# Optimization experiments

Measured on AMD Instinct MI355X. Metric: run time of the kernel, lower is better.

Reference implementation:

```python
import jax, jax.numpy as jnp
from jax import lax
import numpy as np

T, B, H, NUM_DATA, IN_DIM = 2048, 256, 128, 4096, 1


def setup_inputs() -> dict:
    key = jax.random.key(0)
    ks = jax.random.split(key, 9)
    s = 1.0 / np.sqrt(H)  # PyTorch LSTM/Linear default init scale
    inp = {
        "input": jax.random.normal(ks[0], (T, B, IN_DIM), dtype=jnp.float32),
        "label": jax.random.randint(ks[1], (B,), 0, NUM_DATA),
        "h0": jnp.zeros((1, NUM_DATA, H), dtype=jnp.float32),
        "W_ih": jax.random.uniform(ks[2], (4 * H, IN_DIM), jnp.float32, -s, s),
        "W_hh": jax.random.uniform(ks[3], (4 * H, H), jnp.float32, -s, s),
        "b_ih": jax.random.uniform(ks[4], (4 * H,), jnp.float32, -s, s),
        "b_hh": jax.random.uniform(ks[5], (4 * H,), jnp.float32, -s, s),
        "W_lin": jax.random.uniform(ks[6], (IN_DIM, H), jnp.float32, -s, s),
        "b_lin": jax.random.uniform(ks[7], (IN_DIM,), jnp.float32, -s, s),
    }
    return inp


def reference(input, label, h0, W_ih, W_hh, b_ih, b_hh, W_lin, b_lin):
    seq_len = input.shape[0]
    num_in_batch = input.shape[1]
    # Gather learned initial hidden state per sequence id (the python cat loop in torch)
    h = h0[0, label]                                   # (B, H)
    c = jnp.zeros_like(h)                              # (B, H)
    y0 = jnp.zeros((num_in_batch, IN_DIM), input.dtype)  # t=0 input is zeros
    b = b_ih + b_hh                                    # (4H,)

    def step(carry, _):
        h, c, x = carry
        gates = x @ W_ih.T + h @ W_hh.T + b            # (B, 4H); torch gate order i,f,g,o
        i, f, g, o = jnp.split(gates, 4, axis=-1)
        i = jax.nn.sigmoid(i)
        f = jax.nn.sigmoid(f)
        g = jnp.tanh(g)
        o = jax.nn.sigmoid(o)
        c = f * c + i * g
        h = o * jnp.tanh(c)
        y = h @ W_lin.T + b_lin                        # (B, 1) -> fed back as next input
        return (h, c, y), y

    _, ys = lax.scan(step, (h, c, y0), None, length=seq_len)
    return ys  # (T, B, 1), matches torch cat of (1, B, 1) along dim 0
```

## Files before the change

kernel.cpp:

```cpp
#include <hip/hip_runtime.h>
#include <math.h>

#define T_STEPS 2048
#define BATCH   256
#define HDIM    128

__device__ __forceinline__ float fast_rcp(float x) { return __builtin_amdgcn_rcpf(x); }
__device__ __forceinline__ float sigmoid_f(float x) { return fast_rcp(1.0f + __expf(-x)); }
__device__ __forceinline__ float tanh_f(float x) {
    float e = __expf(2.0f * x);
    return 1.0f - 2.0f * fast_rcp(e + 1.0f);
}

#define REP8(M) M(0) M(1) M(2) M(3) M(4) M(5) M(6) M(7)

__global__ __launch_bounds__(512, 2)
void lstm_seq_kernel(const int*   __restrict__ label,
                     const float* __restrict__ h0,
                     const float* __restrict__ W_ih,
                     const float* __restrict__ W_hh,
                     const float* __restrict__ b_ih,
                     const float* __restrict__ b_hh,
                     const float* __restrict__ W_lin,
                     const float* __restrict__ b_lin,
                     float*       __restrict__ out)
{
    const int tid   = threadIdx.x;
    const int batch = blockIdx.x;
    const int m     = tid >> 2;
    const int q     = tid & 3;
    const int q8    = q * 8;

    const int ri = m, rf = m + 128, rg = m + 256, ro = m + 384;

    __shared__ __attribute__((aligned(16))) float hist[128 * 144];

    const float4* W4 = (const float4*)W_hh;
    const float4* L4 = (const float4*)W_lin;

    #define DECL_W(i) \
        float4 wi##i = W4[ri * 32 + q8 + (i)]; \
        float4 wf##i = W4[rf * 32 + q8 + (i)]; \
        float4 wg##i = W4[rg * 32 + q8 + (i)]; \
        float4 wo##i = W4[ro * 32 + q8 + (i)];
    REP8(DECL_W)

    const float wih_i = W_ih[ri], wih_f = W_ih[rf];
    const float wih_g = W_ih[rg], wih_o = W_ih[ro];
    const float blin  = b_lin[0];

    const float bi_ = b_ih[ri] + b_hh[ri] + wih_i * blin;
    const float bf_ = b_ih[rf] + b_hh[rf] + wih_f * blin;
    const float bg_ = b_ih[rg] + b_hh[rg] + wih_g * blin;
    const float bo_ = b_ih[ro] + b_hh[ro] + wih_o * blin;

    const float SNEG = -0x1.715476p+0f;
    const float SG   =  0x1.715476p+1f;
    const float sI = bi_ * 0.25f * SNEG;
    const float sF = bf_ * 0.25f * SNEG;
    const float sG_ = bg_ * 0.25f * SG;
    const float sO = bo_ * 0.25f * SNEG;

    const float b0s = (q==0)?sI :(q==1)?sF :(q==2)?sG_:sO;
    const float b1s = (q==0)?sF :(q==1)?sI :(q==2)?sO :sG_;
    const float b2s = (q==0)?sG_:(q==1)?sO :(q==2)?sI :sF;
    const float b3s = (q==0)?sO :(q==1)?sG_:(q==2)?sF :sI;
    const float wihA = (q==0)?wih_i:(q==1)?wih_f:(q==2)?wih_g:wih_o;
    const float wihB = (q==0)?wih_f:(q==1)?wih_i:(q==2)?wih_o:wih_g;
    const float wihC = (q==0)?wih_g:(q==1)?wih_o:(q==2)?wih_i:wih_f;
    const float wihD = (q==0)?wih_o:(q==1)?wih_g:(q==2)?wih_f:wih_i;
    const float sc0 = ( q     == 2) ? SG : SNEG;
    const float sc1 = ((q^1)  == 2) ? SG : SNEG;
    const float sc2 = ((q^2)  == 2) ? SG : SNEG;
    const float sc3 = ((q^3)  == 2) ? SG : SNEG;
    const float caq = (q==2) ? -2.0f : 1.0f;
    const float cbq = (q==2) ?  1.0f : 0.0f;

    #define FOLD_W(i) { float4 lv = L4[q8 + (i)]; \
        wi##i.x = fmaf(wih_i, lv.x, wi##i.x); wi##i.y = fmaf(wih_i, lv.y, wi##i.y); \
        wi##i.z = fmaf(wih_i, lv.z, wi##i.z); wi##i.w = fmaf(wih_i, lv.w, wi##i.w); \
        wf##i.x = fmaf(wih_f, lv.x, wf##i.x); wf##i.y = fmaf(wih_f, lv.y, wf##i.y); \
        wf##i.z = fmaf(wih_f, lv.z, wf##i.z); wf##i.w = fmaf(wih_f, lv.w, wf##i.w); \
        wg##i.x = fmaf(wih_g, lv.x, wg##i.x); wg##i.y = fmaf(wih_g, lv.y, wg##i.y); \
        wg##i.z = fmaf(wih_g, lv.z, wg##i.z); wg##i.w = fmaf(wih_g, lv.w, wg##i.w); \
        wo##i.x = fmaf(wih_o, lv.x, wo##i.x); wo##i.y = fmaf(wih_o, lv.y, wo##i.y); \
        wo##i.z = fmaf(wih_o, lv.z, wo##i.z); wo##i.w = fmaf(wih_o, lv.w, wo##i.w); }
    REP8(FOLD_W)

    const int   lane = tid & 63;
    const int   ya0w = lane + ((lane >> 5) << 2);
    const float wl_a = W_lin[lane];
    const float wl_b = W_lin[lane + 64];
    const int   hword = m + ((m >> 5) << 2);

    float* slotI = &hist[144 * 127];
    if (tid < HDIM) slotI[tid + ((tid >> 5) << 2)] = h0[label[batch] * HDIM + tid];
    __syncthreads();

    float p0 = slotI[ya0w] * wl_a + slotI[ya0w + 72] * wl_b;
    #pragma unroll
    for (int off = 1; off < 64; off <<= 1) p0 += __shfl_xor(p0, off, 64);
    const float y0 = p0 + blin;

    const float cbi = bi_ - wih_i * y0;
    const float cbf = bf_ - wih_f * y0;
    const float cbg = bg_ - wih_g * y0;
    const float cbo = bo_ - wih_o * y0;

    const float4* hq0 = (const float4*)(slotI + 36 * q);
    float ai = 0.f, af = 0.f, ag = 0.f, ao = 0.f;
    #define DOT4(i) { float4 hv = hq0[(i)]; \
        ai = fmaf(hv.x, wi##i.x, ai); ai = fmaf(hv.y, wi##i.y, ai); \
        ai = fmaf(hv.z, wi##i.z, ai); ai = fmaf(hv.w, wi##i.w, ai); \
        af = fmaf(hv.x, wf##i.x, af); af = fmaf(hv.y, wf##i.y, af); \
        af = fmaf(hv.z, wf##i.z, af); af = fmaf(hv.w, wf##i.w, af); \
        ag = fmaf(hv.x, wg##i.x, ag); ag = fmaf(hv.y, wg##i.y, ag); \
        ag = fmaf(hv.z, wg##i.z, ag); ag = fmaf(hv.w, wg##i.w, ag); \
        ao = fmaf(hv.x, wo##i.x, ao); ao = fmaf(hv.y, wo##i.y, ao); \
        ao = fmaf(hv.z, wo##i.z, ao); ao = fmaf(hv.w, wo##i.w, ao); }
    REP8(DOT4)
    ai += __shfl_xor(ai, 1, 64); af += __shfl_xor(af, 1, 64);
    ag += __shfl_xor(ag, 1, 64); ao += __shfl_xor(ao, 1, 64);
    ai += __shfl_xor(ai, 2, 64); af += __shfl_xor(af, 2, 64);
    ag += __shfl_xor(ag, 2, 64); ao += __shfl_xor(ao, 2, 64);
    const float iv0 = sigmoid_f(ai + cbi);
    const float fv0 = sigmoid_f(af + cbf);
    const float gv0 = tanh_f  (ag + cbg);
    const float ov0 = sigmoid_f(ao + cbo);
    float c = iv0 * gv0;
    const float hn0 = ov0 * tanh_f(c);
    if (q == 0) hist[hword] = hn0;
    __syncthreads();

    const unsigned histB = (unsigned)(unsigned long long)(&hist[0]);
    const unsigned vR0 = histB + 144u * (unsigned)q;
    const unsigned hW0 = histB + 4u * (unsigned)hword;
    const unsigned vD0 = (unsigned)(144 * q - 4 * hword);
    const unsigned fR0 = histB + 576u * (unsigned)m + 144u * (unsigned)q;
    const unsigned jO0 = 1024u * (unsigned)m;
    const unsigned vO0 = 4u * (unsigned)batch;
    const unsigned off0 = (unsigned)((m + 128 * (q    )) * 512 + q * 128);
    const unsigned off1 = (unsigned)((m + 128 * (q ^ 1)) * 512 + q * 128);
    const unsigned off2 = (unsigned)((m + 128 * (q ^ 2)) * 512 + q * 128);
    const unsigned off3 = (unsigned)((m + 128 * (q ^ 3)) * 512 + q * 128);
    const unsigned offL = (unsigned)(q * 128);

    asm volatile(
        "v_mov_b32 v220, %[b0]\n\t"
        "v_mov_b32 v221, 0\n\t"
        "v_mov_b32 v222, %[b1]\n\t"
        "v_mov_b32 v223, 0\n\t"
        "v_mov_b32 v224, %[b2]\n\t"
        "v_mov_b32 v225, 0\n\t"
        "v_mov_b32 v226, %[b3]\n\t"
        "v_mov_b32 v227, 0\n\t"
        "v_mov_b32 v185, %[blin]\n\t"
        "v_mov_b32 v168, %[c0]\n\t"
        "v_mov_b32 v172, %[vR]\n\t"
        "v_mov_b32 v174, %[hW]\n\t"
        "v_mov_b32 v186, %[vD]\n\t"
        "v_mov_b32 v184, %[fR]\n\t"
        "v_mov_b32 v171, %[jO]\n\t"
        "v_mov_b32 v176, %[vO]\n\t"
        "s_mov_b32 s26, 0x11111111\n\t"
        "s_mov_b32 s27, 0x11111111\n\t"
        "global_load_dwordx4 v[32:35], %[off0], %[whh] offset:0\n\t"
        "global_load_dwordx4 v[36:39], %[off0], %[whh] offset:16\n\t"
        "global_load_dwordx4 v[40:43], %[off0], %[whh] offset:32\n\t"
        "global_load_dwordx4 v[44:47], %[off0], %[whh] offset:48\n\t"
        "global_load_dwordx4 v[48:51], %[off0], %[whh] offset:64\n\t"
        "global_load_dwordx4 v[52:55], %[off0], %[whh] offset:80\n\t"
        "global_load_dwordx4 v[56:59], %[off0], %[whh] offset:96\n\t"
        "global_load_dwordx4 v[60:63], %[off0], %[whh] offset:112\n\t"
        "global_load_dwordx4 v[64:67], %[off1], %[whh] offset:0\n\t"
        "global_load_dwordx4 v[68:71], %[off1], %[whh] offset:16\n\t"
        "global_load_dwordx4 v[72:75], %[off1], %[whh] offset:32\n\t"
        "global_load_dwordx4 v[76:79], %[off1], %[whh] offset:48\n\t"
        "global_load_dwordx4 v[80:83], %[off1], %[whh] offset:64\n\t"
        "global_load_dwordx4 v[84:87], %[off1], %[whh] offset:80\n\t"
        "global_load_dwordx4 v[88:91], %[off1], %[whh] offset:96\n\t"
        "global_load_dwordx4 v[92:95], %[off1], %[whh] offset:112\n\t"
        "global_load_dwordx4 v[96:99], %[off2], %[whh] offset:0\n\t"
        "global_load_dwordx4 v[100:103], %[off2], %[whh] offset:16\n\t"
        "global_load_dwordx4 v[104:107], %[off2], %[whh] offset:32\n\t"
        "global_load_dwordx4 v[108:111], %[off2], %[whh] offset:48\n\t"
        "global_load_dwordx4 v[112:115], %[off2], %[whh] offset:64\n\t"
        "global_load_dwordx4 v[116:119], %[off2], %[whh] offset:80\n\t"
        "global_load_dwordx4 v[120:123], %[off2], %[whh] offset:96\n\t"
        "global_load_dwordx4 v[124:127], %[off2], %[whh] offset:112\n\t"
        "global_load_dwordx4 v[128:131], %[off3], %[whh] offset:0\n\t"
        "global_load_dwordx4 v[132:135], %[off3], %[whh] offset:16\n\t"
        "global_load_dwordx4 v[136:139], %[off3], %[whh] offset:32\n\t"
        "global_load_dwordx4 v[140:143], %[off3], %[whh] offset:48\n\t"
        "global_load_dwordx4 v[144:147], %[off3], %[whh] offset:64\n\t"
        "global_load_dwordx4 v[148:151], %[off3], %[whh] offset:80\n\t"
        "global_load_dwordx4 v[152:155], %[off3], %[whh] offset:96\n\t"
        "global_load_dwordx4 v[156:159], %[off3], %[whh] offset:112\n\t"
        "global_load_dwordx4 v[188:191], %[offL], %[wlin] offset:0\n\t"
        "global_load_dwordx4 v[192:195], %[offL], %[wlin] offset:16\n\t"
        "global_load_dwordx4 v[196:199], %[offL], %[wlin] offset:32\n\t"
        "global_load_dwordx4 v[200:203], %[offL], %[wlin] offset:48\n\t"
        "global_load_dwordx4 v[204:207], %[offL], %[wlin] offset:64\n\t"
        "global_load_dwordx4 v[208:211], %[offL], %[wlin] offset:80\n\t"
        "global_load_dwordx4 v[212:215], %[offL], %[wlin] offset:96\n\t"
        "global_load_dwordx4 v[216:219], %[offL], %[wlin] offset:112\n\t"
        "s_waitcnt vmcnt(0)\n\t"
        ".set K_I, 0\n"
        ".rept 32\n"
        " v_fma_f32 v[32+K_I],  %[wA], v[188+K_I], v[32+K_I]\n"
        " v_fma_f32 v[64+K_I],  %[wB], v[188+K_I], v[64+K_I]\n"
        " v_fma_f32 v[96+K_I],  %[wC], v[188+K_I], v[96+K_I]\n"
        " v_fma_f32 v[128+K_I], %[wD], v[188+K_I], v[128+K_I]\n"
        " .set K_I, K_I+1\n"
        ".endr\n"
        ".set K_I, 0\n"
        ".rept 32\n"
        " v_mul_f32 v[32+K_I],  %[sc0], v[32+K_I]\n"
        " v_mul_f32 v[64+K_I],  %[sc1], v[64+K_I]\n"
        " v_mul_f32 v[96+K_I],  %[sc2], v[96+K_I]\n"
        " v_mul_f32 v[128+K_I], %[sc3], v[128+K_I]\n"
        " .set K_I, K_I+1\n"
        ".endr\n"
        "s_movk_i32 s24, 1\n\t"
        "1:\n\t"
        "ds_read_b128 v[0:3],   v172\n\t"
        "ds_read_b128 v[4:7],   v172 offset:16\n\t"
        "ds_read_b128 v[8:11],  v172 offset:32\n\t"
        "ds_read_b128 v[12:15], v172 offset:48\n\t"
        "ds_read_b128 v[16:19], v172 offset:64\n\t"
        "ds_read_b128 v[20:23], v172 offset:80\n\t"
        "ds_read_b128 v[24:27], v172 offset:96\n\t"
        "ds_read_b128 v[28:31], v172 offset:112\n\t"
        "s_waitcnt lgkmcnt(6)\n\t"
        "v_pk_fma_f32 v[160:161], v[0:1], v[32:33], v[220:221]\n\t"
        "v_pk_fma_f32 v[162:163], v[0:1], v[64:65], v[222:223]\n\t"
        "v_pk_fma_f32 v[164:165], v[0:1], v[96:97], v[224:225]\n\t"
        "v_pk_fma_f32 v[166:167], v[0:1], v[128:129], v[226:227]\n\t"
        ".set K_I, 2\n"
        ".rept 3\n"
        " v_pk_fma_f32 v[160:161], v[K_I:K_I+1], v[32+K_I:33+K_I], v[160:161]\n"
        " v_pk_fma_f32 v[162:163], v[K_I:K_I+1], v[64+K_I:65+K_I], v[162:163]\n"
        " v_pk_fma_f32 v[164:165], v[K_I:K_I+1], v[96+K_I:97+K_I], v[164:165]\n"
        " v_pk_fma_f32 v[166:167], v[K_I:K_I+1], v[128+K_I:129+K_I], v[166:167]\n"
        " .set K_I, K_I+2\n"
        ".endr\n"
        "s_waitcnt lgkmcnt(4)\n\t"
        ".rept 4\n"
        " v_pk_fma_f32 v[160:161], v[K_I:K_I+1], v[32+K_I:33+K_I], v[160:161]\n"
        " v_pk_fma_f32 v[162:163], v[K_I:K_I+1], v[64+K_I:65+K_I], v[162:163]\n"
        " v_pk_fma_f32 v[164:165], v[K_I:K_I+1], v[96+K_I:97+K_I], v[164:165]\n"
        " v_pk_fma_f32 v[166:167], v[K_I:K_I+1], v[128+K_I:129+K_I], v[166:167]\n"
        " .set K_I, K_I+2\n"
        ".endr\n"
        "s_waitcnt lgkmcnt(2)\n\t"
        ".rept 4\n"
        " v_pk_fma_f32 v[160:161], v[K_I:K_I+1], v[32+K_I:33+K_I], v[160:161]\n"
        " v_pk_fma_f32 v[162:163], v[K_I:K_I+1], v[64+K_I:65+K_I], v[162:163]\n"
        " v_pk_fma_f32 v[164:165], v[K_I:K_I+1], v[96+K_I:97+K_I], v[164:165]\n"
        " v_pk_fma_f32 v[166:167], v[K_I:K_I+1], v[128+K_I:129+K_I], v[166:167]\n"
        " .set K_I, K_I+2\n"
        ".endr\n"
        "s_waitcnt lgkmcnt(0)\n\t"
        ".rept 4\n"
        " v_pk_fma_f32 v[160:161], v[K_I:K_I+1], v[32+K_I:33+K_I], v[160:161]\n"
        " v_pk_fma_f32 v[162:163], v[K_I:K_I+1], v[64+K_I:65+K_I], v[162:163]\n"
        " v_pk_fma_f32 v[164:165], v[K_I:K_I+1], v[96+K_I:97+K_I], v[164:165]\n"
        " v_pk_fma_f32 v[166:167], v[K_I:K_I+1], v[128+K_I:129+K_I], v[166:167]\n"
        " .set K_I, K_I+2\n"
        ".endr\n"
        "v_add_f32 v160, v160, v161\n\t"
        "v_add_f32 v161, v162, v163\n\t"
        "v_add_f32 v164, v164, v165\n\t"
        "v_add_f32 v165, v166, v167\n\t"
        "s_nop 1\n\t"
        "v_add_f32_dpp v160, v161, v160 quad_perm:[1,0,3,2] row_mask:0xf bank_mask:0xf\n\t"
        "v_add_f32_dpp v164, v165, v164 quad_perm:[1,0,3,2] row_mask:0xf bank_mask:0xf\n\t"
        "v_add_u32 v174, 0x240, v174\n\t"
        "v_add_u32 v172, v174, v186\n\t"
        "s_nop 1\n\t"
        "v_add_f32_dpp v160, v164, v160 quad_perm:[2,3,0,1] row_mask:0xf bank_mask:0xf\n\t"
        "s_nop 3\n\t"
        "v_exp_f32 v160, v160\n\t"
        "s_nop 1\n\t"
        "v_add_f32 v160, 1.0, v160\n\t"
        "v_rcp_f32 v160, v160\n\t"
        "s_nop 1\n\t"
        "v_fma_f32 v166, %[ca], v160, %[cb]\n\t"
        "s_nop 3\n\t"
        "v_mul_f32_dpp v161, v166, v166 quad_perm:[2,3,0,1] row_mask:0xf bank_mask:0xf\n\t"
        "v_mov_b32_dpp v162, v166 quad_perm:[1,0,3,2] row_mask:0xf bank_mask:0xf\n\t"
        "v_mov_b32_dpp v165, v166 quad_perm:[3,3,3,3] row_mask:0xf bank_mask:0xf\n\t"
        "s_nop 2\n\t"
        "v_fma_f32 v168, v162, v168, v161\n\t"
        "v_mul_f32 v163, 0x4038aa3b, v168\n\t"
        "v_exp_f32 v163, v163\n\t"
        "s_nop 1\n\t"
        "v_add_f32 v163, 1.0, v163\n\t"
        "v_rcp_f32 v163, v163\n\t"
        "s_nop 1\n\t"
        "v_fma_f32 v163, -2.0, v163, 1.0\n\t"
        "v_mul_f32 v169, v165, v163\n\t"
        "s_mov_b64 s[22:23], exec\n\t"
        "s_mov_b64 exec, s[26:27]\n\t"
        "ds_write_b32 v174, v169\n\t"
        "s_mov_b64 exec, s[22:23]\n\t"
        "s_waitcnt lgkmcnt(0)\n\t"
        "s_barrier\n\t"
        "s_and_b32 s20, s24, 127\n\t"
        "s_cmp_lg_u32 s20, 127\n\t"
        "s_cbranch_scc1 3f\n\t"
        "v_add_u32 v174, 0xfffee000, v174\n\t"
        "ds_read_b128 v[0:3],   v184\n\t"
        "ds_read_b128 v[4:7],   v184 offset:16\n\t"
        "ds_read_b128 v[8:11],  v184 offset:32\n\t"
        "ds_read_b128 v[12:15], v184 offset:48\n\t"
        "ds_read_b128 v[16:19], v184 offset:64\n\t"
        "ds_read_b128 v[20:23], v184 offset:80\n\t"
        "ds_read_b128 v[24:27], v184 offset:96\n\t"
        "ds_read_b128 v[28:31], v184 offset:112\n\t"
        "v_mov_b32 v164, 0\n\t"
        "s_waitcnt lgkmcnt(0)\n\t"
        ".set K_I, 0\n"
        ".rept 32\n"
        " v_fma_f32 v164, v[0+K_I], v[188+K_I], v164\n"
        " .set K_I, K_I+1\n"
        ".endr\n"
        "s_nop 1\n\t"
        "v_add_f32_dpp v164, v164, v164 quad_perm:[1,0,3,2] row_mask:0xf bank_mask:0xf\n\t"
        "s_nop 1\n\t"
        "v_add_f32_dpp v164, v164, v164 quad_perm:[2,3,0,1] row_mask:0xf bank_mask:0xf\n\t"
        "v_add_f32 v164, v164, v185\n\t"
        "v_add_u32 v170, v176, v171\n\t"
        "s_mov_b64 s[22:23], exec\n\t"
        "s_mov_b64 exec, s[26:27]\n\t"
        "global_store_dword v170, v164, %[outp]\n\t"
        "s_mov_b64 exec, s[22:23]\n\t"
        "v_add_u32 v176, 0x20000, v176\n\t"
        "s_barrier\n\t"
        "3:\n\t"
        "s_add_i32 s24, s24, 1\n\t"
        "s_cmp_lt_i32 s24, 2048\n\t"
        "s_cbranch_scc1 1b\n\t"
        :
        : [off0]"v"(off0), [off1]"v"(off1), [off2]"v"(off2), [off3]"v"(off3),
          [offL]"v"(offL), [whh]"s"(W_hh), [wlin]"s"(W_lin), [outp]"s"(out),
          [wA]"v"(wihA), [wB]"v"(wihB), [wC]"v"(wihC), [wD]"v"(wihD),
          [b0]"v"(b0s), [b1]"v"(b1s), [b2]"v"(b2s), [b3]"v"(b3s),
          [sc0]"v"(sc0), [sc1]"v"(sc1), [sc2]"v"(sc2), [sc3]"v"(sc3),
          [ca]"v"(caq), [cb]"v"(cbq),
          [blin]"s"(blin), [c0]"v"(c),
          [vR]"v"(vR0), [hW]"v"(hW0), [vD]"v"(vD0), [fR]"v"(fR0),
          [jO]"v"(jO0), [vO]"s"(vO0)
        : "memory", "scc", "vcc", "s20","s21","s22","s23","s24","s25","s26","s27",
          "v0","v1","v2","v3","v4","v5","v6","v7","v8","v9",
          "v10","v11","v12","v13","v14","v15","v16","v17","v18","v19",
          "v20","v21","v22","v23","v24","v25","v26","v27","v28","v29",
          "v30","v31","v32","v33","v34","v35","v36","v37","v38","v39",
          "v40","v41","v42","v43","v44","v45","v46","v47","v48","v49",
          "v50","v51","v52","v53","v54","v55","v56","v57","v58","v59",
          "v60","v61","v62","v63","v64","v65","v66","v67","v68","v69",
          "v70","v71","v72","v73","v74","v75","v76","v77","v78","v79",
          "v80","v81","v82","v83","v84","v85","v86","v87","v88","v89",
          "v90","v91","v92","v93","v94","v95","v96","v97","v98","v99",
          "v100","v101","v102","v103","v104","v105","v106","v107","v108","v109",
          "v110","v111","v112","v113","v114","v115","v116","v117","v118","v119",
          "v120","v121","v122","v123","v124","v125","v126","v127","v128","v129",
          "v130","v131","v132","v133","v134","v135","v136","v137","v138","v139",
          "v140","v141","v142","v143","v144","v145","v146","v147","v148","v149",
          "v150","v151","v152","v153","v154","v155","v156","v157","v158","v159",
          "v160","v161","v162","v163","v164","v165","v166","v167","v168","v169",
          "v170","v171","v172","v173","v174","v175","v176","v177","v178","v179",
          "v180","v181","v182","v183","v184","v185","v186","v187","v188","v189",
          "v190","v191","v192","v193","v194","v195","v196","v197","v198","v199",
          "v200","v201","v202","v203","v204","v205","v206","v207","v208","v209",
          "v210","v211","v212","v213","v214","v215","v216","v217","v218","v219",
          "v220","v221","v222","v223","v224","v225","v226","v227");
}

extern "C" void kernel_launch(void* const* d_in, const int* in_sizes, int n_in,
                              void* d_out, int out_size, void* d_ws, size_t ws_size,
                              hipStream_t stream) {
    const int*   label = (const int*)  d_in[1];
    const float* h0    = (const float*)d_in[2];
    const float* W_ih  = (const float*)d_in[3];
    const float* W_hh  = (const float*)d_in[4];
    const float* b_ih  = (const float*)d_in[5];
    const float* b_hh  = (const float*)d_in[6];
    const float* W_lin = (const float*)d_in[7];
    const float* b_lin = (const float*)d_in[8];
    float* out = (float*)d_out;

    lstm_seq_kernel<<<dim3(BATCH), dim3(512), 0, stream>>>(
        label, h0, W_ih, W_hh, b_ih, b_hh, W_lin, b_lin, out);
}
```

Measured before the change: 1.126 ms.

## Split each hidden row's dot product across two lane groups with 1024-thread blocks

The block grows from 512 to 1024 threads. Each of the 4 lanes per hidden row now owns a 16-element slice of the K dimension instead of 32, and the extra row_ror:8 DPP step completes the reduction. This halves the per-thread recurrent dot-product chain and register use per step, and frees enough registers to drop the persistent W_lin copy, which is reloaded from global memory at every 128-step flush instead. The cost is an extra cross-lane reduction stage, a barrier across 16 waves rather than 8, and extra global loads at each flush.

```diff
diff --git a/kernel.cpp b/kernel.cpp
--- a/kernel.cpp
+++ b/kernel.cpp
@@ -12,9 +12,9 @@
     return 1.0f - 2.0f * fast_rcp(e + 1.0f);
 }
 
-#define REP8(M) M(0) M(1) M(2) M(3) M(4) M(5) M(6) M(7)
-
-__global__ __launch_bounds__(512, 2)
+#define REP4(M) M(0) M(1) M(2) M(3)
+
+__global__ __launch_bounds__(1024, 4)
 void lstm_seq_kernel(const int*   __restrict__ label,
                      const float* __restrict__ h0,
                      const float* __restrict__ W_ih,
@@ -27,11 +27,12 @@
 {
     const int tid   = threadIdx.x;
     const int batch = blockIdx.x;
-    const int m     = tid >> 2;
-    const int q     = tid & 3;
-    const int q8    = q * 8;
+    const int q = tid & 3;
+    const int s = (tid >> 3) & 1;
+    const int m = ((tid >> 4) << 1) | ((tid >> 2) & 1);
 
     const int ri = m, rf = m + 128, rg = m + 256, ro = m + 384;
+    const int cb4 = 16 * s + 4 * q;
 
     __shared__ __attribute__((aligned(16))) float hist[128 * 144];
 
@@ -39,11 +40,11 @@
     const float4* L4 = (const float4*)W_lin;
 
     #define DECL_W(i) \
-        float4 wi##i = W4[ri * 32 + q8 + (i)]; \
-        float4 wf##i = W4[rf * 32 + q8 + (i)]; \
-        float4 wg##i = W4[rg * 32 + q8 + (i)]; \
-        float4 wo##i = W4[ro * 32 + q8 + (i)];
-    REP8(DECL_W)
+        float4 wi##i = W4[ri * 32 + cb4 + (i)]; \
+        float4 wf##i = W4[rf * 32 + cb4 + (i)]; \
+        float4 wg##i = W4[rg * 32 + cb4 + (i)]; \
+        float4 wo##i = W4[ro * 32 + cb4 + (i)];
+    REP4(DECL_W)
 
     const float wih_i = W_ih[ri], wih_f = W_ih[rf];
     const float wih_g = W_ih[rg], wih_o = W_ih[ro];
@@ -56,27 +57,22 @@
 
     const float SNEG = -0x1.715476p+0f;
     const float SG   =  0x1.715476p+1f;
-    const float sI = bi_ * 0.25f * SNEG;
-    const float sF = bf_ * 0.25f * SNEG;
-    const float sG_ = bg_ * 0.25f * SG;
-    const float sO = bo_ * 0.25f * SNEG;
-
-    const float b0s = (q==0)?sI :(q==1)?sF :(q==2)?sG_:sO;
-    const float b1s = (q==0)?sF :(q==1)?sI :(q==2)?sO :sG_;
-    const float b2s = (q==0)?sG_:(q==1)?sO :(q==2)?sI :sF;
-    const float b3s = (q==0)?sO :(q==1)?sG_:(q==2)?sF :sI;
+
+    const float bq = (q==0) ? bi_*SNEG : (q==1) ? bf_*SNEG
+                   : (q==2) ? bg_*SG   : bo_*SNEG;
+
     const float wihA = (q==0)?wih_i:(q==1)?wih_f:(q==2)?wih_g:wih_o;
     const float wihB = (q==0)?wih_f:(q==1)?wih_i:(q==2)?wih_o:wih_g;
     const float wihC = (q==0)?wih_g:(q==1)?wih_o:(q==2)?wih_i:wih_f;
     const float wihD = (q==0)?wih_o:(q==1)?wih_g:(q==2)?wih_f:wih_i;
-    const float sc0 = ( q     == 2) ? SG : SNEG;
-    const float sc1 = ((q^1)  == 2) ? SG : SNEG;
-    const float sc2 = ((q^2)  == 2) ? SG : SNEG;
-    const float sc3 = ((q^3)  == 2) ? SG : SNEG;
+    const float sc0 = ( q    == 2) ? SG : SNEG;
+    const float sc1 = ((q^1) == 2) ? SG : SNEG;
+    const float sc2 = ((q^2) == 2) ? SG : SNEG;
+    const float sc3 = ((q^3) == 2) ? SG : SNEG;
     const float caq = (q==2) ? -2.0f : 1.0f;
     const float cbq = (q==2) ?  1.0f : 0.0f;
 
-    #define FOLD_W(i) { float4 lv = L4[q8 + (i)]; \
+    #define FOLD_W(i) { float4 lv = L4[cb4 + (i)]; \
         wi##i.x = fmaf(wih_i, lv.x, wi##i.x); wi##i.y = fmaf(wih_i, lv.y, wi##i.y); \
         wi##i.z = fmaf(wih_i, lv.z, wi##i.z); wi##i.w = fmaf(wih_i, lv.w, wi##i.w); \
         wf##i.x = fmaf(wih_f, lv.x, wf##i.x); wf##i.y = fmaf(wih_f, lv.y, wf##i.y); \
@@ -85,12 +81,12 @@
         wg##i.z = fmaf(wih_g, lv.z, wg##i.z); wg##i.w = fmaf(wih_g, lv.w, wg##i.w); \
         wo##i.x = fmaf(wih_o, lv.x, wo##i.x); wo##i.y = fmaf(wih_o, lv.y, wo##i.y); \
         wo##i.z = fmaf(wih_o, lv.z, wo##i.z); wo##i.w = fmaf(wih_o, lv.w, wo##i.w); }
-    REP8(FOLD_W)
-
-    const int   lane = tid & 63;
-    const int   ya0w = lane + ((lane >> 5) << 2);
-    const float wl_a = W_lin[lane];
-    const float wl_b = W_lin[lane + 64];
+    REP4(FOLD_W)
+
+    const int   lane  = tid & 63;
+    const int   ya0w  = lane + ((lane >> 5) << 2);
+    const float wl_a  = W_lin[lane];
+    const float wl_b  = W_lin[lane + 64];
     const int   hword = m + ((m >> 5) << 2);
 
     float* slotI = &hist[144 * 127];
@@ -107,9 +103,10 @@
     const float cbg = bg_ - wih_g * y0;
     const float cbo = bo_ - wih_o * y0;
 
-    const float4* hq0 = (const float4*)(slotI + 36 * q);
+    const float4* hs = (const float4*)slotI;
+    const int hb4 = 18 * s + 4 * q + (q >> 1);
     float ai = 0.f, af = 0.f, ag = 0.f, ao = 0.f;
-    #define DOT4(i) { float4 hv = hq0[(i)]; \
+    #define DOT4(i) { float4 hv = hs[hb4 + (i)]; \
         ai = fmaf(hv.x, wi##i.x, ai); ai = fmaf(hv.y, wi##i.y, ai); \
         ai = fmaf(hv.z, wi##i.z, ai); ai = fmaf(hv.w, wi##i.w, ai); \
         af = fmaf(hv.x, wf##i.x, af); af = fmaf(hv.y, wf##i.y, af); \
@@ -118,224 +115,184 @@
         ag = fmaf(hv.z, wg##i.z, ag); ag = fmaf(hv.w, wg##i.w, ag); \
         ao = fmaf(hv.x, wo##i.x, ao); ao = fmaf(hv.y, wo##i.y, ao); \
         ao = fmaf(hv.z, wo##i.z, ao); ao = fmaf(hv.w, wo##i.w, ao); }
-    REP8(DOT4)
+    REP4(DOT4)
     ai += __shfl_xor(ai, 1, 64); af += __shfl_xor(af, 1, 64);
     ag += __shfl_xor(ag, 1, 64); ao += __shfl_xor(ao, 1, 64);
     ai += __shfl_xor(ai, 2, 64); af += __shfl_xor(af, 2, 64);
     ag += __shfl_xor(ag, 2, 64); ao += __shfl_xor(ao, 2, 64);
+    ai += __shfl_xor(ai, 8, 64); af += __shfl_xor(af, 8, 64);
+    ag += __shfl_xor(ag, 8, 64); ao += __shfl_xor(ao, 8, 64);
     const float iv0 = sigmoid_f(ai + cbi);
     const float fv0 = sigmoid_f(af + cbf);
     const float gv0 = tanh_f  (ag + cbg);
     const float ov0 = sigmoid_f(ao + cbo);
     float c = iv0 * gv0;
     const float hn0 = ov0 * tanh_f(c);
-    if (q == 0) hist[hword] = hn0;
+    if (q == 0 && s == 0) hist[hword] = hn0;
     __syncthreads();
 
     const unsigned histB = (unsigned)(unsigned long long)(&hist[0]);
-    const unsigned vR0 = histB + 144u * (unsigned)q;
+    const unsigned chunkoff = 288u*(unsigned)s + 64u*(unsigned)q + 16u*(unsigned)(q>>1);
+    const unsigned vR0 = histB + chunkoff;
     const unsigned hW0 = histB + 4u * (unsigned)hword;
-    const unsigned vD0 = (unsigned)(144 * q - 4 * hword);
-    const unsigned fR0 = histB + 576u * (unsigned)m + 144u * (unsigned)q;
+    const unsigned vD0 = chunkoff - 4u * (unsigned)hword;
+    const unsigned fR0 = histB + 576u * (unsigned)m + chunkoff;
     const unsigned jO0 = 1024u * (unsigned)m;
-    const unsigned vO0 = 4u * (unsigned)batch;
-    const unsigned off0 = (unsigned)((m + 128 * (q    )) * 512 + q * 128);
-    const unsigned off1 = (unsigned)((m + 128 * (q ^ 1)) * 512 + q * 128);
-    const unsigned off2 = (unsigned)((m + 128 * (q ^ 2)) * 512 + q * 128);
-    const unsigned off3 = (unsigned)((m + 128 * (q ^ 3)) * 512 + q * 128);
-    const unsigned offL = (unsigned)(q * 128);
+    const unsigned oA0 = 4u * (unsigned)batch;
+    const unsigned off0 = (unsigned)((m + 128 * (q    )) * 512 + 256*s + 64*q);
+    const unsigned off1 = (unsigned)((m + 128 * (q ^ 1)) * 512 + 256*s + 64*q);
+    const unsigned off2 = (unsigned)((m + 128 * (q ^ 2)) * 512 + 256*s + 64*q);
+    const unsigned off3 = (unsigned)((m + 128 * (q ^ 3)) * 512 + 256*s + 64*q);
+    const unsigned offL = (unsigned)(256*s + 64*q);
 
     asm volatile(
-        "v_mov_b32 v220, %[b0]\n\t"
-        "v_mov_b32 v221, 0\n\t"
-        "v_mov_b32 v222, %[b1]\n\t"
-        "v_mov_b32 v223, 0\n\t"
-        "v_mov_b32 v224, %[b2]\n\t"
-        "v_mov_b32 v225, 0\n\t"
-        "v_mov_b32 v226, %[b3]\n\t"
-        "v_mov_b32 v227, 0\n\t"
-        "v_mov_b32 v185, %[blin]\n\t"
-        "v_mov_b32 v168, %[c0]\n\t"
-        "v_mov_b32 v172, %[vR]\n\t"
-        "v_mov_b32 v174, %[hW]\n\t"
-        "v_mov_b32 v186, %[vD]\n\t"
-        "v_mov_b32 v184, %[fR]\n\t"
-        "v_mov_b32 v171, %[jO]\n\t"
-        "v_mov_b32 v176, %[vO]\n\t"
-        "s_mov_b32 s26, 0x11111111\n\t"
-        "s_mov_b32 s27, 0x11111111\n\t"
-        "global_load_dwordx4 v[32:35], %[off0], %[whh] offset:0\n\t"
-        "global_load_dwordx4 v[36:39], %[off0], %[whh] offset:16\n\t"
-        "global_load_dwordx4 v[40:43], %[off0], %[whh] offset:32\n\t"
-        "global_load_dwordx4 v[44:47], %[off0], %[whh] offset:48\n\t"
-        "global_load_dwordx4 v[48:51], %[off0], %[whh] offset:64\n\t"
-        "global_load_dwordx4 v[52:55], %[off0], %[whh] offset:80\n\t"
-        "global_load_dwordx4 v[56:59], %[off0], %[whh] offset:96\n\t"
-        "global_load_dwordx4 v[60:63], %[off0], %[whh] offset:112\n\t"
-        "global_load_dwordx4 v[64:67], %[off1], %[whh] offset:0\n\t"
-        "global_load_dwordx4 v[68:71], %[off1], %[whh] offset:16\n\t"
-        "global_load_dwordx4 v[72:75], %[off1], %[whh] offset:32\n\t"
-        "global_load_dwordx4 v[76:79], %[off1], %[whh] offset:48\n\t"
-        "global_load_dwordx4 v[80:83], %[off1], %[whh] offset:64\n\t"
-        "global_load_dwordx4 v[84:87], %[off1], %[whh] offset:80\n\t"
-        "global_load_dwordx4 v[88:91], %[off1], %[whh] offset:96\n\t"
-        "global_load_dwordx4 v[92:95], %[off1], %[whh] offset:112\n\t"
-        "global_load_dwordx4 v[96:99], %[off2], %[whh] offset:0\n\t"
-        "global_load_dwordx4 v[100:103], %[off2], %[whh] offset:16\n\t"
-        "global_load_dwordx4 v[104:107], %[off2], %[whh] offset:32\n\t"
-        "global_load_dwordx4 v[108:111], %[off2], %[whh] offset:48\n\t"
-        "global_load_dwordx4 v[112:115], %[off2], %[whh] offset:64\n\t"
-        "global_load_dwordx4 v[116:119], %[off2], %[whh] offset:80\n\t"
-        "global_load_dwordx4 v[120:123], %[off2], %[whh] offset:96\n\t"
-        "global_load_dwordx4 v[124:127], %[off2], %[whh] offset:112\n\t"
-        "global_load_dwordx4 v[128:131], %[off3], %[whh] offset:0\n\t"
-        "global_load_dwordx4 v[132:135], %[off3], %[whh] offset:16\n\t"
-        "global_load_dwordx4 v[136:139], %[off3], %[whh] offset:32\n\t"
-        "global_load_dwordx4 v[140:143], %[off3], %[whh] offset:48\n\t"
-        "global_load_dwordx4 v[144:147], %[off3], %[whh] offset:64\n\t"
-        "global_load_dwordx4 v[148:151], %[off3], %[whh] offset:80\n\t"
-        "global_load_dwordx4 v[152:155], %[off3], %[whh] offset:96\n\t"
-        "global_load_dwordx4 v[156:159], %[off3], %[whh] offset:112\n\t"
-        "global_load_dwordx4 v[188:191], %[offL], %[wlin] offset:0\n\t"
-        "global_load_dwordx4 v[192:195], %[offL], %[wlin] offset:16\n\t"
-        "global_load_dwordx4 v[196:199], %[offL], %[wlin] offset:32\n\t"
-        "global_load_dwordx4 v[200:203], %[offL], %[wlin] offset:48\n\t"
-        "global_load_dwordx4 v[204:207], %[offL], %[wlin] offset:64\n\t"
-        "global_load_dwordx4 v[208:211], %[offL], %[wlin] offset:80\n\t"
-        "global_load_dwordx4 v[212:215], %[offL], %[wlin] offset:96\n\t"
-        "global_load_dwordx4 v[216:219], %[offL], %[wlin] offset:112\n\t"
+        "v_mov_b32 v96, %[vR]\n\t"
+        "v_mov_b32 v97, %[hW]\n\t"
+        "v_mov_b32 v98, %[c0]\n\t"
+        "v_mov_b32 v88, 0\n\t"
+        "v_mov_b32 v89, 0\n\t"
+        "s_mov_b32 s26, 0x00110011\n\t"
+        "s_mov_b32 s27, 0x00110011\n\t"
+        "s_mov_b32 s28, %[oA]\n\t"
+        "global_load_dwordx4 v[16:19], %[off0], %[whh] offset:0\n\t"
+        "global_load_dwordx4 v[20:23], %[off0], %[whh] offset:16\n\t"
+        "global_load_dwordx4 v[24:27], %[off0], %[whh] offset:32\n\t"
+        "global_load_dwordx4 v[28:31], %[off0], %[whh] offset:48\n\t"
+        "global_load_dwordx4 v[32:35], %[off1], %[whh] offset:0\n\t"
+        "global_load_dwordx4 v[36:39], %[off1], %[whh] offset:16\n\t"
+        "global_load_dwordx4 v[40:43], %[off1], %[whh] offset:32\n\t"
+        "global_load_dwordx4 v[44:47], %[off1], %[whh] offset:48\n\t"
+        "global_load_dwordx4 v[48:51], %[off2], %[whh] offset:0\n\t"
+        "global_load_dwordx4 v[52:55], %[off2], %[whh] offset:16\n\t"
+        "global_load_dwordx4 v[56:59], %[off2], %[whh] offset:32\n\t"
+        "global_load_dwordx4 v[60:63], %[off2], %[whh] offset:48\n\t"
+        "global_load_dwordx4 v[64:67], %[off3], %[whh] offset:0\n\t"
+        "global_load_dwordx4 v[68:71], %[off3], %[whh] offset:16\n\t"
+        "global_load_dwordx4 v[72:75], %[off3], %[whh] offset:32\n\t"
+        "global_load_dwordx4 v[76:79], %[off3], %[whh] offset:48\n\t"
+        "global_load_dwordx4 v[0:3],   %[offL], %[wlin] offset:0\n\t"
+        "global_load_dwordx4 v[4:7],   %[offL], %[wlin] offset:16\n\t"
+        "global_load_dwordx4 v[8:11],  %[offL], %[wlin] offset:32\n\t"
+        "global_load_dwordx4 v[12:15], %[offL], %[wlin] offset:48\n\t"
         "s_waitcnt vmcnt(0)\n\t"
         ".set K_I, 0\n"
-        ".rept 32\n"
-        " v_fma_f32 v[32+K_I],  %[wA], v[188+K_I], v[32+K_I]\n"
-        " v_fma_f32 v[64+K_I],  %[wB], v[188+K_I], v[64+K_I]\n"
-        " v_fma_f32 v[96+K_I],  %[wC], v[188+K_I], v[96+K_I]\n"
-        " v_fma_f32 v[128+K_I], %[wD], v[188+K_I], v[128+K_I]\n"
+        ".rept 16\n"
+        " v_fma_f32 v[16+K_I], %[wA], v[K_I], v[16+K_I]\n"
+        " v_fma_f32 v[32+K_I], %[wB], v[K_I], v[32+K_I]\n"
+        " v_fma_f32 v[48+K_I], %[wC], v[K_I], v[48+K_I]\n"
+        " v_fma_f32 v[64+K_I], %[wD], v[K_I], v[64+K_I]\n"
         " .set K_I, K_I+1\n"
         ".endr\n"
         ".set K_I, 0\n"
-        ".rept 32\n"
-        " v_mul_f32 v[32+K_I],  %[sc0], v[32+K_I]\n"
-        " v_mul_f32 v[64+K_I],  %[sc1], v[64+K_I]\n"
-        " v_mul_f32 v[96+K_I],  %[sc2], v[96+K_I]\n"
-        " v_mul_f32 v[128+K_I], %[sc3], v[128+K_I]\n"
+        ".rept 16\n"
+        " v_mul_f32 v[16+K_I], %[sc0], v[16+K_I]\n"
+        " v_mul_f32 v[32+K_I], %[sc1], v[32+K_I]\n"
+        " v_mul_f32 v[48+K_I], %[sc2], v[48+K_I]\n"
+        " v_mul_f32 v[64+K_I], %[sc3], v[64+K_I]\n"
         " .set K_I, K_I+1\n"
         ".endr\n"
         "s_movk_i32 s24, 1\n\t"
         "1:\n\t"
-        "ds_read_b128 v[0:3],   v172\n\t"
-        "ds_read_b128 v[4:7],   v172 offset:16\n\t"
-        "ds_read_b128 v[8:11],  v172 offset:32\n\t"
-        "ds_read_b128 v[12:15], v172 offset:48\n\t"
-        "ds_read_b128 v[16:19], v172 offset:64\n\t"
-        "ds_read_b128 v[20:23], v172 offset:80\n\t"
-        "ds_read_b128 v[24:27], v172 offset:96\n\t"
-        "ds_read_b128 v[28:31], v172 offset:112\n\t"
-        "s_waitcnt lgkmcnt(6)\n\t"
-        "v_pk_fma_f32 v[160:161], v[0:1], v[32:33], v[220:221]\n\t"
-        "v_pk_fma_f32 v[162:163], v[0:1], v[64:65], v[222:223]\n\t"
-        "v_pk_fma_f32 v[164:165], v[0:1], v[96:97], v[224:225]\n\t"
-        "v_pk_fma_f32 v[166:167], v[0:1], v[128:129], v[226:227]\n\t"
+        "ds_read_b128 v[0:3],   v96\n\t"
+        "ds_read_b128 v[4:7],   v96 offset:16\n\t"
+        "ds_read_b128 v[8:11],  v96 offset:32\n\t"
+        "ds_read_b128 v[12:15], v96 offset:48\n\t"
+        "s_waitcnt lgkmcnt(2)\n\t"
+        "v_pk_fma_f32 v[80:81], v[0:1], v[16:17], v[88:89]\n\t"
+        "v_pk_fma_f32 v[82:83], v[0:1], v[32:33], v[88:89]\n\t"
+        "v_pk_fma_f32 v[84:85], v[0:1], v[48:49], v[88:89]\n\t"
+        "v_pk_fma_f32 v[86:87], v[0:1], v[64:65], v[88:89]\n\t"
         ".set K_I, 2\n"
         ".rept 3\n"
-        " v_pk_fma_f32 v[160:161], v[K_I:K_I+1], v[32+K_I:33+K_I], v[160:161]\n"
-        " v_pk_fma_f32 v[162:163], v[K_I:K_I+1], v[64+K_I:65+K_I], v[162:163]\n"
-        " v_pk_fma_f32 v[164:165], v[K_I:K_I+1], v[96+K_I:97+K_I], v[164:165]\n"
-        " v_pk_fma_f32 v[166:167], v[K_I:K_I+1], v[128+K_I:129+K_I], v[166:167]\n"
-        " .set K_I, K_I+2\n"
-        ".endr\n"
-        "s_waitcnt lgkmcnt(4)\n\t"
-        ".rept 4\n"
-        " v_pk_fma_f32 v[160:161], v[K_I:K_I+1], v[32+K_I:33+K_I], v[160:161]\n"
-        " v_pk_fma_f32 v[162:163], v[K_I:K_I+1], v[64+K_I:65+K_I], v[162:163]\n"
-        " v_pk_fma_f32 v[164:165], v[K_I:K_I+1], v[96+K_I:97+K_I], v[164:165]\n"
-        " v_pk_fma_f32 v[166:167], v[K_I:K_I+1], v[128+K_I:129+K_I], v[166:167]\n"
-        " .set K_I, K_I+2\n"
-        ".endr\n"
-        "s_waitcnt lgkmcnt(2)\n\t"
-        ".rept 4\n"
-        " v_pk_fma_f32 v[160:161], v[K_I:K_I+1], v[32+K_I:33+K_I], v[160:161]\n"
-        " v_pk_fma_f32 v[162:163], v[K_I:K_I+1], v[64+K_I:65+K_I], v[162:163]\n"
-        " v_pk_fma_f32 v[164:165], v[K_I:K_I+1], v[96+K_I:97+K_I], v[164:165]\n"
-        " v_pk_fma_f32 v[166:167], v[K_I:K_I+1], v[128+K_I:129+K_I], v[166:167]\n"
+        " v_pk_fma_f32 v[80:81], v[K_I:K_I+1], v[16+K_I:17+K_I], v[80:81]\n"
+        " v_pk_fma_f32 v[82:83], v[K_I:K_I+1], v[32+K_I:33+K_I], v[82:83]\n"
+        " v_pk_fma_f32 v[84:85], v[K_I:K_I+1], v[48+K_I:49+K_I], v[84:85]\n"
+        " v_pk_fma_f32 v[86:87], v[K_I:K_I+1], v[64+K_I:65+K_I], v[86:87]\n"
         " .set K_I, K_I+2\n"
         ".endr\n"
         "s_waitcnt lgkmcnt(0)\n\t"
         ".rept 4\n"
-        " v_pk_fma_f32 v[160:161], v[K_I:K_I+1], v[32+K_I:33+K_I], v[160:161]\n"
-        " v_pk_fma_f32 v[162:163], v[K_I:K_I+1], v[64+K_I:65+K_I], v[162:163]\n"
-        " v_pk_fma_f32 v[164:165], v[K_I:K_I+1], v[96+K_I:97+K_I], v[164:165]\n"
-        " v_pk_fma_f32 v[166:167], v[K_I:K_I+1], v[128+K_I:129+K_I], v[166:167]\n"
+        " v_pk_fma_f32 v[80:81], v[K_I:K_I+1], v[16+K_I:17+K_I], v[80:81]\n"
+        " v_pk_fma_f32 v[82:83], v[K_I:K_I+1], v[32+K_I:33+K_I], v[82:83]\n"
+        " v_pk_fma_f32 v[84:85], v[K_I:K_I+1], v[48+K_I:49+K_I], v[84:85]\n"
+        " v_pk_fma_f32 v[86:87], v[K_I:K_I+1], v[64+K_I:65+K_I], v[86:87]\n"
         " .set K_I, K_I+2\n"
         ".endr\n"
-        "v_add_f32 v160, v160, v161\n\t"
-        "v_add_f32 v161, v162, v163\n\t"
-        "v_add_f32 v164, v164, v165\n\t"
-        "v_add_f32 v165, v166, v167\n\t"
-        "s_nop 1\n\t"
-        "v_add_f32_dpp v160, v161, v160 quad_perm:[1,0,3,2] row_mask:0xf bank_mask:0xf\n\t"
-        "v_add_f32_dpp v164, v165, v164 quad_perm:[1,0,3,2] row_mask:0xf bank_mask:0xf\n\t"
-        "v_add_u32 v174, 0x240, v174\n\t"
-        "v_add_u32 v172, v174, v186\n\t"
-        "s_nop 1\n\t"
-        "v_add_f32_dpp v160, v164, v160 quad_perm:[2,3,0,1] row_mask:0xf bank_mask:0xf\n\t"
+        "v_add_f32 v80, v80, v81\n\t"
+        "v_add_f32 v81, v82, v83\n\t"
+        "v_add_f32 v84, v84, v85\n\t"
+        "v_add_f32 v85, v86, v87\n\t"
+        "s_nop 1\n\t"
+        "v_add_f32_dpp v80, v81, v80 quad_perm:[1,0,3,2] row_mask:0xf bank_mask:0xf\n\t"
+        "v_add_f32_dpp v84, v85, v84 quad_perm:[1,0,3,2] row_mask:0xf bank_mask:0xf\n\t"
+        "v_add_u32 v97, 0x240, v97\n\t"
+        "v_add_u32 v96, v97, %[vD]\n\t"
+        "v_add_f32_dpp v80, v84, v80 quad_perm:[2,3,0,1] row_mask:0xf bank_mask:0xf\n\t"
+        "s_nop 1\n\t"
+        "v_add_f32_dpp v80, v80, v80 row_ror:8 row_mask:0xf bank_mask:0xf\n\t"
+        "s_nop 2\n\t"
+        "v_add_f32 v80, %[bq], v80\n\t"
+        "v_exp_f32 v80, v80\n\t"
+        "s_nop 1\n\t"
+        "v_add_f32 v80, 1.0, v80\n\t"
+        "v_rcp_f32 v80, v80\n\t"
+        "s_nop 1\n\t"
+        "v_fma_f32 v90, %[ca], v80, %[cb]\n\t"
         "s_nop 3\n\t"
-        "v_exp_f32 v160, v160\n\t"
-        "s_nop 1\n\t"
-        "v_add_f32 v160, 1.0, v160\n\t"
-        "v_rcp_f32 v160, v160\n\t"
-        "s_nop 1\n\t"
-        "v_fma_f32 v166, %[ca], v160, %[cb]\n\t"
-        "s_nop 3\n\t"
-        "v_mul_f32_dpp v161, v166, v166 quad_perm:[2,3,0,1] row_mask:0xf bank_mask:0xf\n\t"
-        "v_mov_b32_dpp v162, v166 quad_perm:[1,0,3,2] row_mask:0xf bank_mask:0xf\n\t"
-        "v_mov_b32_dpp v165, v166 quad_perm:[3,3,3,3] row_mask:0xf bank_mask:0xf\n\t"
+        "v_mul_f32_dpp v91, v90, v90 quad_perm:[2,3,0,1] row_mask:0xf bank_mask:0xf\n\t"
+        "v_mov_b32_dpp v92, v90 quad_perm:[1,0,3,2] row_mask:0xf bank_mask:0xf\n\t"
+        "v_mov_b32_dpp v93, v90 quad_perm:[3,3,3,3] row_mask:0xf bank_mask:0xf\n\t"
         "s_nop 2\n\t"
-        "v_fma_f32 v168, v162, v168, v161\n\t"
-        "v_mul_f32 v163, 0x4038aa3b, v168\n\t"
-        "v_exp_f32 v163, v163\n\t"
-        "s_nop 1\n\t"
-        "v_add_f32 v163, 1.0, v163\n\t"
-        "v_rcp_f32 v163, v163\n\t"
-        "s_nop 1\n\t"
-        "v_fma_f32 v163, -2.0, v163, 1.0\n\t"
-        "v_mul_f32 v169, v165, v163\n\t"
+        "v_fma_f32 v98, v92, v98, v91\n\t"
+        "v_mul_f32 v94, 0x4038aa3b, v98\n\t"
+        "v_exp_f32 v94, v94\n\t"
+        "s_nop 1\n\t"
+        "v_add_f32 v94, 1.0, v94\n\t"
+        "v_rcp_f32 v94, v94\n\t"
+        "s_nop 1\n\t"
+        "v_fma_f32 v94, -2.0, v94, 1.0\n\t"
+        "v_mul_f32 v99, v93, v94\n\t"
         "s_mov_b64 s[22:23], exec\n\t"
         "s_mov_b64 exec, s[26:27]\n\t"
-        "ds_write_b32 v174, v169\n\t"
+        "ds_write_b32 v97, v99\n\t"
         "s_mov_b64 exec, s[22:23]\n\t"
         "s_waitcnt lgkmcnt(0)\n\t"
         "s_barrier\n\t"
         "s_and_b32 s20, s24, 127\n\t"
         "s_cmp_lg_u32 s20, 127\n\t"
         "s_cbranch_scc1 3f\n\t"
-        "v_add_u32 v174, 0xfffee000, v174\n\t"
-        "ds_read_b128 v[0:3],   v184\n\t"
-        "ds_read_b128 v[4:7],   v184 offset:16\n\t"
-        "ds_read_b128 v[8:11],  v184 offset:32\n\t"
-        "ds_read_b128 v[12:15], v184 offset:48\n\t"
-        "ds_read_b128 v[16:19], v184 offset:64\n\t"
-        "ds_read_b128 v[20:23], v184 offset:80\n\t"
-        "ds_read_b128 v[24:27], v184 offset:96\n\t"
-        "ds_read_b128 v[28:31], v184 offset:112\n\t"
-        "v_mov_b32 v164, 0\n\t"
-        "s_waitcnt lgkmcnt(0)\n\t"
+        "v_add_u32 v97, 0xfffee000, v97\n\t"
+        "global_load_dwordx4 v[80:83], %[offL], %[wlin] offset:0\n\t"
+        "global_load_dwordx4 v[84:87], %[offL], %[wlin] offset:16\n\t"
+        "global_load_dwordx4 v[88:91], %[offL], %[wlin] offset:32\n\t"
+        "global_load_dwordx4 v[92:95], %[offL], %[wlin] offset:48\n\t"
+        "ds_read_b128 v[0:3],   %[fR]\n\t"
+        "ds_read_b128 v[4:7],   %[fR] offset:16\n\t"
+        "ds_read_b128 v[8:11],  %[fR] offset:32\n\t"
+        "ds_read_b128 v[12:15], %[fR] offset:48\n\t"
+        "v_mov_b32 v100, 0\n\t"
+        "s_waitcnt vmcnt(0) lgkmcnt(0)\n\t"
         ".set K_I, 0\n"
-        ".rept 32\n"
-        " v_fma_f32 v164, v[0+K_I], v[188+K_I], v164\n"
+        ".rept 16\n"
+        " v_fma_f32 v100, v[K_I], v[80+K_I], v100\n"
         " .set K_I, K_I+1\n"
         ".endr\n"
         "s_nop 1\n\t"
-        "v_add_f32_dpp v164, v164, v164 quad_perm:[1,0,3,2] row_mask:0xf bank_mask:0xf\n\t"
-        "s_nop 1\n\t"
-        "v_add_f32_dpp v164, v164, v164 quad_perm:[2,3,0,1] row_mask:0xf bank_mask:0xf\n\t"
-        "v_add_f32 v164, v164, v185\n\t"
-        "v_add_u32 v170, v176, v171\n\t"
+        "v_add_f32_dpp v100, v100, v100 quad_perm:[1,0,3,2] row_mask:0xf bank_mask:0xf\n\t"
+        "s_nop 1\n\t"
+        "v_add_f32_dpp v100, v100, v100 quad_perm:[2,3,0,1] row_mask:0xf bank_mask:0xf\n\t"
+        "s_nop 1\n\t"
+        "v_add_f32_dpp v100, v100, v100 row_ror:8 row_mask:0xf bank_mask:0xf\n\t"
+        "s_nop 2\n\t"
+        "v_add_f32 v100, %[blinS], v100\n\t"
+        "v_add_u32 v101, s28, %[jO]\n\t"
         "s_mov_b64 s[22:23], exec\n\t"
         "s_mov_b64 exec, s[26:27]\n\t"
-        "global_store_dword v170, v164, %[outp]\n\t"
+        "global_store_dword v101, v100, %[outp]\n\t"
         "s_mov_b64 exec, s[22:23]\n\t"
-        "v_add_u32 v176, 0x20000, v176\n\t"
+        "s_add_u32 s28, s28, 0x20000\n\t"
+        "v_mov_b32 v88, 0\n\t"
+        "v_mov_b32 v89, 0\n\t"
         "s_barrier\n\t"
         "3:\n\t"
         "s_add_i32 s24, s24, 1\n\t"
@@ -345,13 +302,13 @@
         : [off0]"v"(off0), [off1]"v"(off1), [off2]"v"(off2), [off3]"v"(off3),
           [offL]"v"(offL), [whh]"s"(W_hh), [wlin]"s"(W_lin), [outp]"s"(out),
           [wA]"v"(wihA), [wB]"v"(wihB), [wC]"v"(wihC), [wD]"v"(wihD),
-          [b0]"v"(b0s), [b1]"v"(b1s), [b2]"v"(b2s), [b3]"v"(b3s),
           [sc0]"v"(sc0), [sc1]"v"(sc1), [sc2]"v"(sc2), [sc3]"v"(sc3),
-          [ca]"v"(caq), [cb]"v"(cbq),
-          [blin]"s"(blin), [c0]"v"(c),
+          [bq]"v"(bq), [ca]"v"(caq), [cb]"v"(cbq),
+          [blinS]"s"(blin), [c0]"v"(c),
           [vR]"v"(vR0), [hW]"v"(hW0), [vD]"v"(vD0), [fR]"v"(fR0),
-          [jO]"v"(jO0), [vO]"s"(vO0)
-        : "memory", "scc", "vcc", "s20","s21","s22","s23","s24","s25","s26","s27",
+          [jO]"v"(jO0), [oA]"s"(oA0)
+        : "memory", "scc", "vcc",
+          "s20","s21","s22","s23","s24","s25","s26","s27","s28",
           "v0","v1","v2","v3","v4","v5","v6","v7","v8","v9",
           "v10","v11","v12","v13","v14","v15","v16","v17","v18","v19",
           "v20","v21","v22","v23","v24","v25","v26","v27","v28","v29",
@@ -362,19 +319,7 @@
           "v70","v71","v72","v73","v74","v75","v76","v77","v78","v79",
           "v80","v81","v82","v83","v84","v85","v86","v87","v88","v89",
           "v90","v91","v92","v93","v94","v95","v96","v97","v98","v99",
-          "v100","v101","v102","v103","v104","v105","v106","v107","v108","v109",
-          "v110","v111","v112","v113","v114","v115","v116","v117","v118","v119",
-          "v120","v121","v122","v123","v124","v125","v126","v127","v128","v129",
-          "v130","v131","v132","v133","v134","v135","v136","v137","v138","v139",
-          "v140","v141","v142","v143","v144","v145","v146","v147","v148","v149",
-          "v150","v151","v152","v153","v154","v155","v156","v157","v158","v159",
-          "v160","v161","v162","v163","v164","v165","v166","v167","v168","v169",
-          "v170","v171","v172","v173","v174","v175","v176","v177","v178","v179",
-          "v180","v181","v182","v183","v184","v185","v186","v187","v188","v189",
-          "v190","v191","v192","v193","v194","v195","v196","v197","v198","v199",
-          "v200","v201","v202","v203","v204","v205","v206","v207","v208","v209",
-          "v210","v211","v212","v213","v214","v215","v216","v217","v218","v219",
-          "v220","v221","v222","v223","v224","v225","v226","v227");
+          "v100","v101");
 }
 
 extern "C" void kernel_launch(void* const* d_in, const int* in_sizes, int n_in,
@@ -390,6 +335,6 @@
     const float* b_lin = (const float*)d_in[8];
     float* out = (float*)d_out;
 
-    lstm_seq_kernel<<<dim3(BATCH), dim3(512), 0, stream>>>(
+    lstm_seq_kernel<<<dim3(BATCH), dim3(1024), 0, stream>>>(
         label, h0, W_ih, W_hh, b_ih, b_hh, W_lin, b_lin, out);
 }
```

Result: slower. 1.324 ms (+17.6%).
